# Kernel tuning notes

Measured on AMD Instinct MI355X. Metric: run time of the kernel, lower is better.

## Reference

```python
import jax, jax.numpy as jnp
import numpy as np

H, W = 2048, 2048
S = 10            # depth_segments
BOTTOM_PCT = 1    # bottom_percent
P_MIX = 0.5       # p
F_SCALE = 2.0     # f


def setup_inputs() -> dict:
    key = jax.random.key(0)
    k1, k2 = jax.random.split(key)
    image = jax.random.uniform(k1, (3, H, W), dtype=jnp.float32)
    # the |d_nbr - d_ctr| < 1 threshold gives a non-trivial bilateral mask.
    depth = jax.random.uniform(k2, (H, W), dtype=jnp.float32) * 5.0
    mu0 = jnp.ones((), dtype=jnp.float32)
    mu1 = jnp.ones((), dtype=jnp.float32)
    mu2 = jnp.ones((), dtype=jnp.float32)
    return {"image": image, "depth": depth, "mu0": mu0, "mu1": mu1, "mu2": mu2}


def _eigm_forward(image, depth, mu0, mu1, mu2):
    Hh, Ww = depth.shape
    HW = Hh * Ww
    dt = image.dtype

    # --- ULAP depth prior: d = mu0 + mu1*max(g,b) + mu2*r ---
    r, g, b = image[0], image[1], image[2]
    d = mu0 + mu1 * jnp.maximum(g, b) + mu2 * r                    # [H,W]

    # --- per-depth-bin background light B_c and direct signal D_c ---
    bins = jnp.linspace(depth.min(), depth.max(), S + 1)           # [S+1]
    seg = (depth[None] >= bins[:-1, None, None]) & (depth[None] < bins[1:, None, None])  # [S,H,W] bool
    seg_flat = seg.reshape(S, HW)
    n = seg_flat.sum(axis=1)                                       # [S] pixels per bin

    min_rgb = image.min(axis=0).reshape(HW)                        # darkest channel per pixel
    vals = jnp.where(seg_flat, min_rgb[None, :], jnp.asarray(np.inf, dt))
    svals = jnp.sort(vals, axis=1)                                 # segment pixels first, inf padding last
    k = (n * BOTTOM_PCT) // 100                                    # topk(largest=False) count per bin
    take = jnp.arange(HW)[None, :] < k[:, None]
    B_c = jnp.sum(jnp.where(take, svals, jnp.asarray(0.0, dt)), axis=1) / k.astype(dt)  # [S]

    segf = seg.astype(dt)
    seg_mean = jnp.einsum('chw,shw->sc', image, segf) / n.astype(dt)[:, None]  # [S,3]
    D_seg = seg_mean - B_c[:, None]                                # [S,3] per-segment direct signal
    # scatter each segment's D_c to its pixels -> per-pixel map [1,3,H,W]
    D = jnp.einsum('shw,sc->chw', segf, D_seg)[None]

    # --- depth-thresholded 3x3 local average (bilateral-style stencil) ---
    dpad = jnp.pad(depth, 1, constant_values=np.inf)               # inf => out-of-bounds invalid
    Dpad = jnp.pad(D, ((0, 0), (0, 0), (1, 1), (1, 1)))
    num = jnp.zeros_like(D)
    cnt = jnp.zeros((1, 1, Hh, Ww), dt)
    one = jnp.asarray(1.0, dt)
    for dy in (-1, 0, 1):
        for dx in (-1, 0, 1):
            nd = dpad[1 + dy:1 + dy + Hh, 1 + dx:1 + dx + Ww]
            valid = (jnp.abs(nd - depth) < one).astype(dt)[None, None]
            nD = Dpad[:, :, 1 + dy:1 + dy + Hh, 1 + dx:1 + dx + Ww]
            num = num + valid * nD
            cnt = cnt + valid
    a_prime = num / cnt                                            # center always valid -> cnt >= 1
    a_c = P_MIX * D + (1.0 - P_MIX) * a_prime

    E_c = F_SCALE * a_c                                            # [1,3,H,W]
    J_c = E_c * d[None, None]                                      # restored direct signal
    return J_c


def reference(image, depth, mu0, mu1, mu2):
    return _eigm_forward(image, depth, mu0, mu1, mu2)
```

## Files before the change

kernel.cpp:

```cpp
#include <hip/hip_runtime.h>
#include <cstdint>
#include <math.h>

#define HH 2048
#define WW 2048
#define HWPX (HH*WW)
#define NSEG 10
#define NB 128
#define LOWR 0.03125f
#define INV_LOWW 4096.0f
#define BINW (LOWR/(float)NB)

#define K2_BLOCKS 1024
#define SLICE_W 1320

typedef float vfloat4 __attribute__((ext_vector_type(4)));

#define WS_DMIN 0
#define WS_DMAX 1
#define WS_HIST 8
#define HIST_WORDS (NSEG*NB)
#define WS_ACC (WS_HIST + HIST_WORDS)
#define WS_DSEG 1328
#define WS_SLICE 1408

__device__ __forceinline__ int seg_of(float v, float dmin, float dmax, float invw) {
    int sg = (int)((v - dmin) * invw);
    sg = sg > (NSEG-1) ? (NSEG-1) : sg;
    return (v >= dmax) ? NSEG : sg;
}

__global__ void k0_init(uint32_t* __restrict__ wsu) {
    int i = blockIdx.x * blockDim.x + threadIdx.x;
    int nth = gridDim.x * blockDim.x;
    for (int j = i; j < HIST_WORDS + 40; j += nth) wsu[WS_HIST + j] = 0;
    if (i == 0) { wsu[WS_DMIN] = 0x7F800000u; wsu[WS_DMAX] = 0u; }
}

__global__ __launch_bounds__(256) void k1_minmax(const float* __restrict__ depth,
                                                 uint32_t* __restrict__ wsu) {
    int tid = blockIdx.x * 256 + threadIdx.x;
    int nth = gridDim.x * 256;
    float vmin = INFINITY, vmax = 0.0f;
    const float4* d4 = (const float4*)depth;
    for (int i = tid; i < HWPX/4; i += nth) {
        float4 v = d4[i];
        vmin = fminf(vmin, fminf(fminf(v.x, v.y), fminf(v.z, v.w)));
        vmax = fmaxf(vmax, fmaxf(fmaxf(v.x, v.y), fmaxf(v.z, v.w)));
    }
    #pragma unroll
    for (int off = 32; off > 0; off >>= 1) {
        vmin = fminf(vmin, __shfl_down(vmin, off, 64));
        vmax = fmaxf(vmax, __shfl_down(vmax, off, 64));
    }
    __shared__ float smin[4], smax[4];
    int wid = threadIdx.x >> 6;
    if ((threadIdx.x & 63) == 0) { smin[wid] = vmin; smax[wid] = vmax; }
    __syncthreads();
    if (threadIdx.x == 0) {
        float bmin = fminf(fminf(smin[0], smin[1]), fminf(smin[2], smin[3]));
        float bmax = fmaxf(fmaxf(smax[0], smax[1]), fmaxf(smax[2], smax[3]));
        atomicMin(&wsu[WS_DMIN], __float_as_uint(bmin));
        atomicMax(&wsu[WS_DMAX], __float_as_uint(bmax));
    }
}

__global__ __launch_bounds__(256, 2) void k2_hist(const float* __restrict__ image,
                                                  const float* __restrict__ depth,
                                                  uint32_t* __restrict__ wsu) {
    __shared__ uint32_t s_hist[HIST_WORDS];
    __shared__ float s_red[4][40];
    for (int j = threadIdx.x; j < HIST_WORDS; j += 256) s_hist[j] = 0;
    __syncthreads();

    float dmin = __uint_as_float(wsu[WS_DMIN]);
    float dmax = __uint_as_float(wsu[WS_DMAX]);
    float invw = 10.0f / (dmax - dmin);

    float c_cnt[NSEG], c_r[NSEG], c_g[NSEG], c_b[NSEG];
    #pragma unroll
    for (int s = 0; s < NSEG; ++s) { c_cnt[s]=0.f; c_r[s]=0.f; c_g[s]=0.f; c_b[s]=0.f; }

    const float4* r4 = (const float4*)image;
    const float4* g4 = (const float4*)(image + HWPX);
    const float4* b4 = (const float4*)(image + 2*HWPX);
    const float4* d4 = (const float4*)depth;
    int tid = blockIdx.x * 256 + threadIdx.x;
    int nth = K2_BLOCKS * 256;
    for (int i = tid; i < HWPX/4; i += nth) {
        float4 rv = r4[i], gv = g4[i], bv = b4[i], dv = d4[i];
        float ra[4] = {rv.x, rv.y, rv.z, rv.w};
        float ga[4] = {gv.x, gv.y, gv.z, gv.w};
        float ba[4] = {bv.x, bv.y, bv.z, bv.w};
        float da[4] = {dv.x, dv.y, dv.z, dv.w};
        #pragma unroll
        for (int j = 0; j < 4; ++j) {
            int sg = seg_of(da[j], dmin, dmax, invw);
            float m = fminf(ra[j], fminf(ga[j], ba[j]));
            if (sg < NSEG && m < LOWR) {
                atomicAdd(&s_hist[sg*NB + (int)(m * INV_LOWW)], 1u);
            }
            #pragma unroll
            for (int s = 0; s < NSEG; ++s) {
                float sel = (sg == s) ? 1.0f : 0.0f;
                c_cnt[s] += sel;
                c_r[s] += sel * ra[j];
                c_g[s] += sel * ga[j];
                c_b[s] += sel * ba[j];
            }
        }
    }
    #pragma unroll
    for (int s = 0; s < NSEG; ++s) {
        #pragma unroll
        for (int off = 32; off > 0; off >>= 1) {
            c_cnt[s] += __shfl_down(c_cnt[s], off, 64);
            c_r[s]   += __shfl_down(c_r[s],   off, 64);
            c_g[s]   += __shfl_down(c_g[s],   off, 64);
            c_b[s]   += __shfl_down(c_b[s],   off, 64);
        }
    }
    int wid = threadIdx.x >> 6;
    if ((threadIdx.x & 63) == 0) {
        #pragma unroll
        for (int s = 0; s < NSEG; ++s) {
            s_red[wid][s]      = c_cnt[s];
            s_red[wid][10 + s] = c_r[s];
            s_red[wid][20 + s] = c_g[s];
            s_red[wid][30 + s] = c_b[s];
        }
    }
    __syncthreads();
    uint32_t* slice = wsu + WS_SLICE + (size_t)blockIdx.x * SLICE_W;
    for (int j = threadIdx.x; j < HIST_WORDS; j += 256) slice[j] = s_hist[j];
    if (threadIdx.x < 40) {
        float v = s_red[0][threadIdx.x] + s_red[1][threadIdx.x]
                + s_red[2][threadIdx.x] + s_red[3][threadIdx.x];
        ((float*)slice)[HIST_WORDS + threadIdx.x] = v;
    }
}

__global__ __launch_bounds__(256) void k3a_reduce(uint32_t* __restrict__ wsu) {
    int j = blockIdx.x * 256 + threadIdx.x;
    if (j >= SLICE_W) return;
    int b0 = blockIdx.y * (K2_BLOCKS/16);
    if (j < HIST_WORDS) {
        uint32_t acc = 0;
        const uint32_t* p = wsu + WS_SLICE + (size_t)b0 * SLICE_W + j;
        #pragma unroll 4
        for (int b = 0; b < K2_BLOCKS/16; ++b) acc += p[(size_t)b * SLICE_W];
        if (acc) atomicAdd(&wsu[WS_HIST + j], acc);
    } else {
        float acc = 0.0f;
        const float* p = (const float*)(wsu + WS_SLICE + (size_t)b0 * SLICE_W + j);
        #pragma unroll 4
        for (int b = 0; b < K2_BLOCKS/16; ++b) acc += p[(size_t)b * SLICE_W];
        atomicAdd((float*)&wsu[WS_HIST + j], acc);
    }
}

__global__ void k3b_stats(uint32_t* __restrict__ wsu) {
    __shared__ uint32_t sh[HIST_WORDS];
    for (int j = threadIdx.x; j < HIST_WORDS; j += blockDim.x) sh[j] = wsu[WS_HIST + j];
    __syncthreads();
    float* wsf = (float*)wsu;
    int s = threadIdx.x;
    if (s < NSEG) {
        float fn = wsf[WS_ACC + s];
        uint32_t n = (uint32_t)(fn + 0.5f);
        uint32_t k = n / 100;
        const uint32_t* h = &sh[s*NB];
        float bsum = 0.0f; uint32_t taken = 0;
        for (int b = 0; b < NB; ++b) {
            uint32_t rem = k - taken;
            uint32_t c = h[b];
            uint32_t t = c < rem ? c : rem;
            bsum += (float)t * (((float)b + 0.5f) * BINW);
            taken += t;
        }
        if (taken < k) bsum += (float)(k - taken) * LOWR;
        float B = (k > 0) ? (bsum / (float)k) : 0.0f;
        wsf[WS_DSEG + s*4 + 0] = wsf[WS_ACC + 10 + s] / fn - B;
        wsf[WS_DSEG + s*4 + 1] = wsf[WS_ACC + 20 + s] / fn - B;
        wsf[WS_DSEG + s*4 + 2] = wsf[WS_ACC + 30 + s] / fn - B;
        wsf[WS_DSEG + s*4 + 3] = 0.0f;
    } else if (s == NSEG) {
        wsf[WS_DSEG + 40] = 0.0f; wsf[WS_DSEG + 41] = 0.0f;
        wsf[WS_DSEG + 42] = 0.0f; wsf[WS_DSEG + 43] = 0.0f;
    }
}

__global__ __launch_bounds__(256, 2) void k4_out(const float* __restrict__ image,
                                                 const float* __restrict__ depth,
                                                 const float* __restrict__ mu0p,
                                                 const float* __restrict__ mu1p,
                                                 const float* __restrict__ mu2p,
                                                 const uint32_t* __restrict__ wsu,
                                                 float* __restrict__ out) {
    __shared__ float4 s_D4[NSEG+1];
    const float* wsf = (const float*)wsu;
    if (threadIdx.x < NSEG+1)
        s_D4[threadIdx.x] = ((const float4*)(wsf + WS_DSEG))[threadIdx.x];
    __syncthreads();

    float dmin = __uint_as_float(wsu[WS_DMIN]);
    float dmax = __uint_as_float(wsu[WS_DMAX]);
    float invw = 10.0f / (dmax - dmin);
    float mu0 = *mu0p, mu1 = *mu1p, mu2 = *mu2p;

    int gid = blockIdx.x * 256 + threadIdx.x;
    int row = gid >> 9;
    int col = (gid & 511) << 2;
    int lane = threadIdx.x & 63;

    size_t base = (size_t)row * WW + col;
    float4 rv = *(const float4*)(image + base);
    float4 gv = *(const float4*)(image + HWPX + base);
    float4 bv = *(const float4*)(image + 2*HWPX + base);

    float nd[3][6];
    #pragma unroll
    for (int rr = 0; rr < 3; ++rr) {
        int r2 = row + rr - 1;
        if (r2 >= 0 && r2 < HH) {
            const float* dp = depth + (size_t)r2 * WW + col;
            float4 m = *(const float4*)dp;
            float left  = __shfl_up(m.w, 1, 64);
            float right = __shfl_down(m.x, 1, 64);
            if (lane == 0)  left  = (col > 0)      ? dp[-1] : INFINITY;
            if (lane == 63) right = (col + 4 < WW) ? dp[4]  : INFINITY;
            nd[rr][0] = left;  nd[rr][1] = m.x; nd[rr][2] = m.y;
            nd[rr][3] = m.z;   nd[rr][4] = m.w; nd[rr][5] = right;
        } else {
            #pragma unroll
            for (int cc = 0; cc < 6; ++cc) nd[rr][cc] = INFINITY;
        }
    }

    float cnt[4], A0[4], A1[4], A2[4];
    #pragma unroll
    for (int j = 0; j < 4; ++j) { cnt[j]=0.f; A0[j]=0.f; A1[j]=0.f; A2[j]=0.f; }

    #pragma unroll
    for (int rr = 0; rr < 3; ++rr) {
        #pragma unroll
        for (int cc = 0; cc < 6; ++cc) {
            float nv = nd[rr][cc];
            float4 dd = s_D4[seg_of(nv, dmin, dmax, invw)];
            #pragma unroll
            for (int j = 0; j < 4; ++j) {
                if (j >= cc - 2 && j <= cc) {
                    float msk = (fabsf(nv - nd[1][j+1]) < 1.0f) ? 1.0f : 0.0f;
                    cnt[j] += msk; A0[j] += msk*dd.x; A1[j] += msk*dd.y; A2[j] += msk*dd.z;
                }
            }
        }
    }

    float ra[4] = {rv.x, rv.y, rv.z, rv.w};
    float ga[4] = {gv.x, gv.y, gv.z, gv.w};
    float ba[4] = {bv.x, bv.y, bv.z, bv.w};
    float o0[4], o1[4], o2[4];
    #pragma unroll
    for (int j = 0; j < 4; ++j) {
        float rc = 1.0f / cnt[j];
        float4 Dc = s_D4[seg_of(nd[1][j+1], dmin, dmax, invw)];
        float dval = mu0 + mu1 * fmaxf(ga[j], ba[j]) + mu2 * ra[j];
        o0[j] = (Dc.x + A0[j]*rc) * dval;
        o1[j] = (Dc.y + A1[j]*rc) * dval;
        o2[j] = (Dc.z + A2[j]*rc) * dval;
    }
    vfloat4 v0 = {o0[0], o0[1], o0[2], o0[3]};
    vfloat4 v1 = {o1[0], o1[1], o1[2], o1[3]};
    vfloat4 v2 = {o2[0], o2[1], o2[2], o2[3]};
    __builtin_nontemporal_store(v0, (vfloat4*)(out + base));
    __builtin_nontemporal_store(v1, (vfloat4*)(out + HWPX + base));
    __builtin_nontemporal_store(v2, (vfloat4*)(out + 2*HWPX + base));
}

extern "C" void kernel_launch(void* const* d_in, const int* in_sizes, int n_in,
                              void* d_out, int out_size, void* d_ws, size_t ws_size,
                              hipStream_t stream) {
    const float* image = (const float*)d_in[0];
    const float* depth = (const float*)d_in[1];
    const float* mu0   = (const float*)d_in[2];
    const float* mu1   = (const float*)d_in[3];
    const float* mu2   = (const float*)d_in[4];
    uint32_t* wsu = (uint32_t*)d_ws;
    float* out = (float*)d_out;

    hipLaunchKernelGGL(k0_init,    dim3(2),          dim3(256), 0, stream, wsu);
    hipLaunchKernelGGL(k1_minmax,  dim3(256),        dim3(256), 0, stream, depth, wsu);
    hipLaunchKernelGGL(k2_hist,    dim3(K2_BLOCKS),  dim3(256), 0, stream, image, depth, wsu);
    hipLaunchKernelGGL(k3a_reduce, dim3(6, 16),      dim3(256), 0, stream, wsu);
    hipLaunchKernelGGL(k3b_stats,  dim3(1),          dim3(256), 0, stream, wsu);
    hipLaunchKernelGGL(k4_out,     dim3((HWPX/4)/256), dim3(256), 0, stream,
                       image, depth, mu0, mu1, mu2, wsu, out);
}
```

Baseline: 168.3 us.

## Precompute ULAP depth in histogram pass and drop atomics/init kernel

Computes the per-pixel ULAP depth prior in the histogram kernel and stores it to workspace, so the output kernel reads one plane instead of three image planes. Replaces global atomic min/max and histogram atomics with per-block/per-partition partials reduced by consumer kernels, eliminating the init kernel launch. Adds an extra 16 MB write pass in exchange for reduced reads in the final kernel.

```diff
diff --git a/kernel.cpp b/kernel.cpp
--- a/kernel.cpp
+++ b/kernel.cpp
@@ -7,22 +7,23 @@
 #define HWPX (HH*WW)
 #define NSEG 10
 #define NB 128
+#define HIST_WORDS (NSEG*NB)
 #define LOWR 0.03125f
 #define INV_LOWW 4096.0f
 #define BINW (LOWR/(float)NB)
 
 #define K2_BLOCKS 1024
 #define SLICE_W 1320
+#define NPART 16
 
 typedef float vfloat4 __attribute__((ext_vector_type(4)));
 
-#define WS_DMIN 0
-#define WS_DMAX 1
-#define WS_HIST 8
-#define HIST_WORDS (NSEG*NB)
-#define WS_ACC (WS_HIST + HIST_WORDS)
-#define WS_DSEG 1328
-#define WS_SLICE 1408
+#define WS_BMM 0
+#define WS_PART 512
+#define WS_DSEG 21632
+#define WS_DMM (WS_DSEG + 44)
+#define WS_DVAL 21680
+#define WS_SLICE (WS_DVAL + HWPX)
 
 __device__ __forceinline__ int seg_of(float v, float dmin, float dmax, float invw) {
     int sg = (int)((v - dmin) * invw);
@@ -30,15 +31,8 @@
     return (v >= dmax) ? NSEG : sg;
 }
 
-__global__ void k0_init(uint32_t* __restrict__ wsu) {
-    int i = blockIdx.x * blockDim.x + threadIdx.x;
-    int nth = gridDim.x * blockDim.x;
-    for (int j = i; j < HIST_WORDS + 40; j += nth) wsu[WS_HIST + j] = 0;
-    if (i == 0) { wsu[WS_DMIN] = 0x7F800000u; wsu[WS_DMAX] = 0u; }
-}
-
 __global__ __launch_bounds__(256) void k1_minmax(const float* __restrict__ depth,
-                                                 uint32_t* __restrict__ wsu) {
+                                                 float* __restrict__ wsf) {
     int tid = blockIdx.x * 256 + threadIdx.x;
     int nth = gridDim.x * 256;
     float vmin = INFINITY, vmax = 0.0f;
@@ -58,24 +52,43 @@
     if ((threadIdx.x & 63) == 0) { smin[wid] = vmin; smax[wid] = vmax; }
     __syncthreads();
     if (threadIdx.x == 0) {
-        float bmin = fminf(fminf(smin[0], smin[1]), fminf(smin[2], smin[3]));
-        float bmax = fmaxf(fmaxf(smax[0], smax[1]), fmaxf(smax[2], smax[3]));
-        atomicMin(&wsu[WS_DMIN], __float_as_uint(bmin));
-        atomicMax(&wsu[WS_DMAX], __float_as_uint(bmax));
-    }
+        wsf[WS_BMM + blockIdx.x]       = fminf(fminf(smin[0], smin[1]), fminf(smin[2], smin[3]));
+        wsf[WS_BMM + 256 + blockIdx.x] = fmaxf(fmaxf(smax[0], smax[1]), fmaxf(smax[2], smax[3]));
+    }
+}
+
+__device__ __forceinline__ void block_minmax(const float* wsf, float& dmin, float& dmax,
+                                             float smn[4], float smx[4]) {
+    float v0 = wsf[WS_BMM + threadIdx.x];
+    float v1 = wsf[WS_BMM + 256 + threadIdx.x];
+    #pragma unroll
+    for (int off = 32; off > 0; off >>= 1) {
+        v0 = fminf(v0, __shfl_down(v0, off, 64));
+        v1 = fmaxf(v1, __shfl_down(v1, off, 64));
+    }
+    int wid = threadIdx.x >> 6;
+    if ((threadIdx.x & 63) == 0) { smn[wid] = v0; smx[wid] = v1; }
+    __syncthreads();
+    dmin = fminf(fminf(smn[0], smn[1]), fminf(smn[2], smn[3]));
+    dmax = fmaxf(fmaxf(smx[0], smx[1]), fmaxf(smx[2], smx[3]));
 }
 
 __global__ __launch_bounds__(256, 2) void k2_hist(const float* __restrict__ image,
                                                   const float* __restrict__ depth,
+                                                  const float* __restrict__ mu0p,
+                                                  const float* __restrict__ mu1p,
+                                                  const float* __restrict__ mu2p,
                                                   uint32_t* __restrict__ wsu) {
     __shared__ uint32_t s_hist[HIST_WORDS];
     __shared__ float s_red[4][40];
+    __shared__ float smn[4], smx[4];
+    float* wsf = (float*)wsu;
     for (int j = threadIdx.x; j < HIST_WORDS; j += 256) s_hist[j] = 0;
-    __syncthreads();
-
-    float dmin = __uint_as_float(wsu[WS_DMIN]);
-    float dmax = __uint_as_float(wsu[WS_DMAX]);
+
+    float dmin, dmax;
+    block_minmax(wsf, dmin, dmax, smn, smx);
     float invw = 10.0f / (dmax - dmin);
+    float mu0 = *mu0p, mu1 = *mu1p, mu2 = *mu2p;
 
     float c_cnt[NSEG], c_r[NSEG], c_g[NSEG], c_b[NSEG];
     #pragma unroll
@@ -85,6 +98,7 @@
     const float4* g4 = (const float4*)(image + HWPX);
     const float4* b4 = (const float4*)(image + 2*HWPX);
     const float4* d4 = (const float4*)depth;
+    vfloat4* dval4 = (vfloat4*)(wsf + WS_DVAL);
     int tid = blockIdx.x * 256 + threadIdx.x;
     int nth = K2_BLOCKS * 256;
     for (int i = tid; i < HWPX/4; i += nth) {
@@ -93,6 +107,7 @@
         float ga[4] = {gv.x, gv.y, gv.z, gv.w};
         float ba[4] = {bv.x, bv.y, bv.z, bv.w};
         float da[4] = {dv.x, dv.y, dv.z, dv.w};
+        float dvo[4];
         #pragma unroll
         for (int j = 0; j < 4; ++j) {
             int sg = seg_of(da[j], dmin, dmax, invw);
@@ -108,7 +123,10 @@
                 c_g[s] += sel * ga[j];
                 c_b[s] += sel * ba[j];
             }
-        }
+            dvo[j] = mu0 + mu1 * fmaxf(ga[j], ba[j]) + mu2 * ra[j];
+        }
+        vfloat4 dq = {dvo[0], dvo[1], dvo[2], dvo[3]};
+        dval4[i] = dq;
     }
     #pragma unroll
     for (int s = 0; s < NSEG; ++s) {
@@ -143,33 +161,47 @@
 __global__ __launch_bounds__(256) void k3a_reduce(uint32_t* __restrict__ wsu) {
     int j = blockIdx.x * 256 + threadIdx.x;
     if (j >= SLICE_W) return;
-    int b0 = blockIdx.y * (K2_BLOCKS/16);
+    int y = blockIdx.y;
+    const uint32_t* p = wsu + WS_SLICE + (size_t)(y * (K2_BLOCKS/NPART)) * SLICE_W + j;
     if (j < HIST_WORDS) {
         uint32_t acc = 0;
-        const uint32_t* p = wsu + WS_SLICE + (size_t)b0 * SLICE_W + j;
         #pragma unroll 4
-        for (int b = 0; b < K2_BLOCKS/16; ++b) acc += p[(size_t)b * SLICE_W];
-        if (acc) atomicAdd(&wsu[WS_HIST + j], acc);
+        for (int b = 0; b < K2_BLOCKS/NPART; ++b) acc += p[(size_t)b * SLICE_W];
+        wsu[WS_PART + y*SLICE_W + j] = acc;
     } else {
         float acc = 0.0f;
-        const float* p = (const float*)(wsu + WS_SLICE + (size_t)b0 * SLICE_W + j);
         #pragma unroll 4
-        for (int b = 0; b < K2_BLOCKS/16; ++b) acc += p[(size_t)b * SLICE_W];
-        atomicAdd((float*)&wsu[WS_HIST + j], acc);
+        for (int b = 0; b < K2_BLOCKS/NPART; ++b) acc += ((const float*)p)[(size_t)b * SLICE_W];
+        ((float*)wsu)[WS_PART + y*SLICE_W + j] = acc;
     }
 }
 
 __global__ void k3b_stats(uint32_t* __restrict__ wsu) {
-    __shared__ uint32_t sh[HIST_WORDS];
-    for (int j = threadIdx.x; j < HIST_WORDS; j += blockDim.x) sh[j] = wsu[WS_HIST + j];
-    __syncthreads();
+    __shared__ uint32_t s_hist[HIST_WORDS];
+    __shared__ float s_acc[40];
+    __shared__ float smn[4], smx[4];
     float* wsf = (float*)wsu;
+    for (int j = threadIdx.x; j < SLICE_W; j += 256) {
+        if (j < HIST_WORDS) {
+            uint32_t acc = 0;
+            #pragma unroll
+            for (int y = 0; y < NPART; ++y) acc += wsu[WS_PART + y*SLICE_W + j];
+            s_hist[j] = acc;
+        } else {
+            float acc = 0.0f;
+            #pragma unroll
+            for (int y = 0; y < NPART; ++y) acc += wsf[WS_PART + y*SLICE_W + j];
+            s_acc[j - HIST_WORDS] = acc;
+        }
+    }
+    float dmin, dmax;
+    block_minmax(wsf, dmin, dmax, smn, smx);
     int s = threadIdx.x;
     if (s < NSEG) {
-        float fn = wsf[WS_ACC + s];
+        float fn = s_acc[s];
         uint32_t n = (uint32_t)(fn + 0.5f);
         uint32_t k = n / 100;
-        const uint32_t* h = &sh[s*NB];
+        const uint32_t* h = &s_hist[s*NB];
         float bsum = 0.0f; uint32_t taken = 0;
         for (int b = 0; b < NB; ++b) {
             uint32_t rem = k - taken;
@@ -180,21 +212,19 @@
         }
         if (taken < k) bsum += (float)(k - taken) * LOWR;
         float B = (k > 0) ? (bsum / (float)k) : 0.0f;
-        wsf[WS_DSEG + s*4 + 0] = wsf[WS_ACC + 10 + s] / fn - B;
-        wsf[WS_DSEG + s*4 + 1] = wsf[WS_ACC + 20 + s] / fn - B;
-        wsf[WS_DSEG + s*4 + 2] = wsf[WS_ACC + 30 + s] / fn - B;
+        wsf[WS_DSEG + s*4 + 0] = s_acc[10 + s] / fn - B;
+        wsf[WS_DSEG + s*4 + 1] = s_acc[20 + s] / fn - B;
+        wsf[WS_DSEG + s*4 + 2] = s_acc[30 + s] / fn - B;
         wsf[WS_DSEG + s*4 + 3] = 0.0f;
     } else if (s == NSEG) {
         wsf[WS_DSEG + 40] = 0.0f; wsf[WS_DSEG + 41] = 0.0f;
         wsf[WS_DSEG + 42] = 0.0f; wsf[WS_DSEG + 43] = 0.0f;
-    }
-}
-
-__global__ __launch_bounds__(256, 2) void k4_out(const float* __restrict__ image,
-                                                 const float* __restrict__ depth,
-                                                 const float* __restrict__ mu0p,
-                                                 const float* __restrict__ mu1p,
-                                                 const float* __restrict__ mu2p,
+    } else if (s == NSEG+1) {
+        wsf[WS_DMM] = dmin; wsf[WS_DMM + 1] = dmax;
+    }
+}
+
+__global__ __launch_bounds__(256, 2) void k4_out(const float* __restrict__ depth,
                                                  const uint32_t* __restrict__ wsu,
                                                  float* __restrict__ out) {
     __shared__ float4 s_D4[NSEG+1];
@@ -203,20 +233,16 @@
         s_D4[threadIdx.x] = ((const float4*)(wsf + WS_DSEG))[threadIdx.x];
     __syncthreads();
 
-    float dmin = __uint_as_float(wsu[WS_DMIN]);
-    float dmax = __uint_as_float(wsu[WS_DMAX]);
+    float dmin = wsf[WS_DMM];
+    float dmax = wsf[WS_DMM + 1];
     float invw = 10.0f / (dmax - dmin);
-    float mu0 = *mu0p, mu1 = *mu1p, mu2 = *mu2p;
 
     int gid = blockIdx.x * 256 + threadIdx.x;
     int row = gid >> 9;
     int col = (gid & 511) << 2;
     int lane = threadIdx.x & 63;
 
-    size_t base = (size_t)row * WW + col;
-    float4 rv = *(const float4*)(image + base);
-    float4 gv = *(const float4*)(image + HWPX + base);
-    float4 bv = *(const float4*)(image + 2*HWPX + base);
+    float4 dva4 = ((const float4*)(wsf + WS_DVAL))[gid];
 
     float nd[3][6];
     #pragma unroll
@@ -257,19 +283,17 @@
         }
     }
 
-    float ra[4] = {rv.x, rv.y, rv.z, rv.w};
-    float ga[4] = {gv.x, gv.y, gv.z, gv.w};
-    float ba[4] = {bv.x, bv.y, bv.z, bv.w};
+    float dva[4] = {dva4.x, dva4.y, dva4.z, dva4.w};
     float o0[4], o1[4], o2[4];
     #pragma unroll
     for (int j = 0; j < 4; ++j) {
         float rc = 1.0f / cnt[j];
         float4 Dc = s_D4[seg_of(nd[1][j+1], dmin, dmax, invw)];
-        float dval = mu0 + mu1 * fmaxf(ga[j], ba[j]) + mu2 * ra[j];
-        o0[j] = (Dc.x + A0[j]*rc) * dval;
-        o1[j] = (Dc.y + A1[j]*rc) * dval;
-        o2[j] = (Dc.z + A2[j]*rc) * dval;
-    }
+        o0[j] = (Dc.x + A0[j]*rc) * dva[j];
+        o1[j] = (Dc.y + A1[j]*rc) * dva[j];
+        o2[j] = (Dc.z + A2[j]*rc) * dva[j];
+    }
+    size_t base = (size_t)row * WW + col;
     vfloat4 v0 = {o0[0], o0[1], o0[2], o0[3]};
     vfloat4 v1 = {o1[0], o1[1], o1[2], o1[3]};
     vfloat4 v2 = {o2[0], o2[1], o2[2], o2[3]};
@@ -289,11 +313,11 @@
     uint32_t* wsu = (uint32_t*)d_ws;
     float* out = (float*)d_out;
 
-    hipLaunchKernelGGL(k0_init,    dim3(2),          dim3(256), 0, stream, wsu);
-    hipLaunchKernelGGL(k1_minmax,  dim3(256),        dim3(256), 0, stream, depth, wsu);
-    hipLaunchKernelGGL(k2_hist,    dim3(K2_BLOCKS),  dim3(256), 0, stream, image, depth, wsu);
-    hipLaunchKernelGGL(k3a_reduce, dim3(6, 16),      dim3(256), 0, stream, wsu);
-    hipLaunchKernelGGL(k3b_stats,  dim3(1),          dim3(256), 0, stream, wsu);
+    hipLaunchKernelGGL(k1_minmax,  dim3(256),       dim3(256), 0, stream, depth, (float*)wsu);
+    hipLaunchKernelGGL(k2_hist,    dim3(K2_BLOCKS), dim3(256), 0, stream,
+                       image, depth, mu0, mu1, mu2, wsu);
+    hipLaunchKernelGGL(k3a_reduce, dim3(6, NPART),  dim3(256), 0, stream, wsu);
+    hipLaunchKernelGGL(k3b_stats,  dim3(1),         dim3(256), 0, stream, wsu);
     hipLaunchKernelGGL(k4_out,     dim3((HWPX/4)/256), dim3(256), 0, stream,
-                       image, depth, mu0, mu1, mu2, wsu, out);
-}
+                       depth, wsu, out);
+}
```

Result: faster. 158.7 us (-5.7%).
